# Performance work log

Measured on AMD Instinct MI355X. Metric: run time of the kernel, lower is better.

Reference implementation:

```python
import jax, jax.numpy as jnp
import numpy as np

B, N, C = 16, 1024, 768
H, HD = 9, 64  # num_active_heads, head_dim


def setup_inputs() -> dict:
    key = jax.random.key(0)
    ks = jax.random.split(key, 5)
    x = jax.random.normal(ks[0], (B, N, C), dtype=jnp.float32)
    qkv_w = jax.random.normal(ks[1], (3 * H * HD, C), dtype=jnp.float32) * (1.0 / np.sqrt(C))
    qkv_b = jax.random.normal(ks[2], (3 * H * HD,), dtype=jnp.float32) * 0.02
    proj_w = jax.random.normal(ks[3], (C, H * HD), dtype=jnp.float32) * (1.0 / np.sqrt(H * HD))
    proj_b = jax.random.normal(ks[4], (C,), dtype=jnp.float32) * 0.02
    return {"x": x, "qkv_w": qkv_w, "qkv_b": qkv_b, "proj_w": proj_w, "proj_b": proj_b}


def reference(x, qkv_w, qkv_b, proj_w, proj_b):
    b, n, c = x.shape
    # qkv projection: [B,N,3*H*HD] -> [3,B,H,N,HD]
    qkv = (x @ qkv_w.T + qkv_b).reshape(b, n, 3, H, HD).transpose(2, 0, 3, 1, 4)
    q, k, v = qkv[0], qkv[1], qkv[2]
    scale = HD ** -0.5
    attn = jnp.einsum('bhqd,bhkd->bhqk', q, k) * scale  # [B,H,N,N]
    attn = jax.nn.softmax(attn, axis=-1)
    out = jnp.einsum('bhqk,bhkd->bhqd', attn, v)  # [B,H,N,HD]
    out = out.transpose(0, 2, 1, 3).reshape(b, n, H * HD)
    return out @ proj_w.T + proj_b
```

## Files before the change

### kernel.cpp

```cpp
#include <hip/hip_runtime.h>


typedef _Float16 f16x8 __attribute__((ext_vector_type(8)));
typedef _Float16 f16x4 __attribute__((ext_vector_type(4)));
typedef float    f32x4 __attribute__((ext_vector_type(4)));

#define MFMA16(a, b, c) __builtin_amdgcn_mfma_f32_16x16x32_f16(a, b, c, 0, 0, 0)

__global__ __launch_bounds__(256) void cvt_f32_f16(const float* __restrict__ src,
                                                   _Float16* __restrict__ dst,
                                                   int nsrc, int ntot) {
  const int i4 = (blockIdx.x * 256 + threadIdx.x) * 4;
  if (i4 >= ntot) return;
  f16x4 h;
  if (i4 + 4 <= nsrc) {
    const float4 v = *(const float4*)(src + i4);
    ((_Float16*)&h)[0] = (_Float16)v.x;
    ((_Float16*)&h)[1] = (_Float16)v.y;
    ((_Float16*)&h)[2] = (_Float16)v.z;
    ((_Float16*)&h)[3] = (_Float16)v.w;
  } else {
    #pragma unroll
    for (int j = 0; j < 4; ++j) {
      const float v = (i4 + j < nsrc) ? src[i4 + j] : 0.f;
      ((_Float16*)&h)[j] = (_Float16)v;
    }
  }
  *(f16x4*)(dst + i4) = h;
}

__global__ __launch_bounds__(256, 2) void gemm1_qkv(const _Float16* __restrict__ A,
                                                    const _Float16* __restrict__ Bw,
                                                    const float* __restrict__ bias,
                                                    _Float16* __restrict__ Qo,
                                                    _Float16* __restrict__ Ko,
                                                    _Float16* __restrict__ Vt) {
  __shared__ __align__(16) _Float16 As[128 * 72];
  __shared__ __align__(16) _Float16 Bs[128 * 72];
  const int tid = threadIdx.x;
  const int wave = tid >> 6, lane = tid & 63;
  const int lo = lane & 15, hi = lane >> 4;
  const int wm = (wave >> 1) * 64, wn = (wave & 1) * 64;
  const int m0 = blockIdx.x * 128, n0 = blockIdx.y * 128;
  f32x4 acc[4][4] = {};
  for (int k0 = 0; k0 < 768; k0 += 64) {
    __syncthreads();
    #pragma unroll
    for (int it = 0; it < 4; ++it) {
      const int c = it * 256 + tid;
      const int row = c >> 3, cc = c & 7;
      *(uint4*)(As + row * 72 + cc * 8) = *(const uint4*)(A + (m0 + row) * 768 + k0 + cc * 8);
      *(uint4*)(Bs + row * 72 + cc * 8) = *(const uint4*)(Bw + (n0 + row) * 768 + k0 + cc * 8);
    }
    __syncthreads();
    #pragma unroll
    for (int ks = 0; ks < 2; ++ks) {
      f16x8 af[4], bf[4];
      #pragma unroll
      for (int t = 0; t < 4; ++t) {
        af[t] = *(const f16x8*)(As + (wm + t * 16 + lo) * 72 + ks * 32 + hi * 8);
        bf[t] = *(const f16x8*)(Bs + (wn + t * 16 + lo) * 72 + ks * 32 + hi * 8);
      }
      #pragma unroll
      for (int mt = 0; mt < 4; ++mt)
        #pragma unroll
        for (int nt = 0; nt < 4; ++nt)
          acc[mt][nt] = MFMA16(af[mt], bf[nt], acc[mt][nt]);
    }
  }
  const int b = m0 >> 10;
  const int nrbase = (m0 & 1023) + wm;
  #pragma unroll
  for (int nt = 0; nt < 4; ++nt) {
    const int n = n0 + wn + nt * 16 + lo;
    if (n < 1728) {
      const float bv = bias[n];
      const int t3 = n / 576;
      const int rem = n - t3 * 576;
      const int hh = rem >> 6, d = rem & 63;
      if (t3 == 2) {
        _Float16* dv = Vt + ((b * 9 + hh) << 16) + d * 1024;
        #pragma unroll
        for (int mt = 0; mt < 4; ++mt) {
          const int nr = nrbase + mt * 16 + hi * 4;
          f16x4 h4;
          #pragma unroll
          for (int i = 0; i < 4; ++i)
            ((_Float16*)&h4)[i] = (_Float16)(acc[mt][nt][i] + bv);
          *(f16x4*)(dv + nr) = h4;
        }
      } else {
        _Float16* dst = (t3 == 0 ? Qo : Ko) + ((b * 9 + hh) << 16) + d;
        #pragma unroll
        for (int mt = 0; mt < 4; ++mt) {
          const int nr = nrbase + mt * 16 + hi * 4;
          #pragma unroll
          for (int i = 0; i < 4; ++i)
            dst[(nr + i) * 64] = (_Float16)(acc[mt][nt][i] + bv);
        }
      }
    }
  }
}

__global__ __launch_bounds__(256, 3) void attn_fused(const _Float16* __restrict__ Qg,
                                                     const _Float16* __restrict__ Kg,
                                                     const _Float16* __restrict__ Vtg,
                                                     _Float16* __restrict__ Og) {
  __shared__ __align__(16) _Float16 Ks[128 * 72];
  __shared__ __align__(16) _Float16 Vts[64 * 136];
  __shared__ __align__(16) _Float16 QPs[4][16 * 136];
  const int tid = threadIdx.x;
  const int wave = tid >> 6, lane = tid & 63;
  const int lo = lane & 15, hi = lane >> 4;
  const int bh = blockIdx.x;
  const int q0 = blockIdx.y * 64;
  const _Float16* Qp  = Qg + (bh << 16);
  const _Float16* Kp  = Kg + (bh << 16);
  const _Float16* Vtp = Vtg + (bh << 16);

  {
    _Float16* Qs = &QPs[0][0];
    #pragma unroll
    for (int it = 0; it < 2; ++it) {
      const int c = it * 256 + tid;
      const int row = c >> 3, cc = c & 7;
      *(uint4*)(Qs + row * 72 + cc * 8) = *(const uint4*)(Qp + (q0 + row) * 64 + cc * 8);
    }
  }
  __syncthreads();
  f16x8 qf[2];
  #pragma unroll
  for (int ks = 0; ks < 2; ++ks)
    qf[ks] = *(const f16x8*)(&QPs[0][0] + (wave * 16 + lo) * 72 + ks * 32 + hi * 8);

  float m_run = -1e30f, l_run = 0.f;
  f32x4 accO[4] = {};
  const float cs = 0.125f * 1.44269504f;

  for (int t0 = 0; t0 < 1024; t0 += 128) {
    __syncthreads();
    #pragma unroll
    for (int it = 0; it < 4; ++it) {
      const int c = it * 256 + tid;
      const int row = c >> 3, cc = c & 7;
      *(uint4*)(Ks + row * 72 + cc * 8) = *(const uint4*)(Kp + (t0 + row) * 64 + cc * 8);
    }
    #pragma unroll
    for (int it = 0; it < 4; ++it) {
      const int c = it * 256 + tid;
      const int dr = c >> 4, c16 = c & 15;
      *(uint4*)(Vts + dr * 136 + c16 * 8) = *(const uint4*)(Vtp + dr * 1024 + t0 + c16 * 8);
    }
    __syncthreads();

    f32x4 sacc[8] = {};
    #pragma unroll
    for (int tt = 0; tt < 8; ++tt)
      #pragma unroll
      for (int ks = 0; ks < 2; ++ks) {
        const f16x8 kf = *(const f16x8*)(Ks + (tt * 16 + lo) * 72 + ks * 32 + hi * 8);
        sacc[tt] = MFMA16(kf, qf[ks], sacc[tt]);
      }

    float rmax = -1e30f;
    #pragma unroll
    for (int tt = 0; tt < 8; ++tt)
      #pragma unroll
      for (int i = 0; i < 4; ++i)
        rmax = fmaxf(rmax, sacc[tt][i]);
    rmax = fmaxf(rmax, __shfl_xor(rmax, 16, 64));
    rmax = fmaxf(rmax, __shfl_xor(rmax, 32, 64));
    const float mnew = fmaxf(m_run, rmax * cs);
    const float alpha = exp2f(m_run - mnew);
    float rsum = 0.f;
    #pragma unroll
    for (int tt = 0; tt < 8; ++tt) {
      f16x4 ph;
      #pragma unroll
      for (int i = 0; i < 4; ++i) {
        const float p = exp2f(fmaf(sacc[tt][i], cs, -mnew));
        rsum += p;
        ((_Float16*)&ph)[i] = (_Float16)p;
      }
      *(f16x4*)(&QPs[wave][lo * 136 + tt * 16 + hi * 4]) = ph;
    }
    rsum += __shfl_xor(rsum, 16, 64);
    rsum += __shfl_xor(rsum, 32, 64);
    l_run = l_run * alpha + rsum;
    m_run = mnew;
    #pragma unroll
    for (int dt = 0; dt < 4; ++dt) accO[dt] *= alpha;

    #pragma unroll
    for (int ks2 = 0; ks2 < 4; ++ks2) {
      const f16x8 pf = *(const f16x8*)(&QPs[wave][lo * 136 + ks2 * 32 + hi * 8]);
      #pragma unroll
      for (int dt = 0; dt < 4; ++dt) {
        const f16x8 vf = *(const f16x8*)(Vts + (dt * 16 + lo) * 136 + ks2 * 32 + hi * 8);
        accO[dt] = MFMA16(vf, pf, accO[dt]);
      }
    }
  }
  const float inv = 1.f / l_run;
  const int qrow = q0 + wave * 16 + lo;
  const int b = bh / 9, hh = bh - (bh / 9) * 9;
  _Float16* op = Og + (((b << 10) + qrow) * 576 + hh * 64);
  #pragma unroll
  for (int dt = 0; dt < 4; ++dt) {
    f16x4 o4;
    #pragma unroll
    for (int i = 0; i < 4; ++i)
      ((_Float16*)&o4)[i] = (_Float16)(accO[dt][i] * inv);
    *(f16x4*)(op + dt * 16 + hi * 4) = o4;
  }
}

__global__ __launch_bounds__(256, 2) void gemm3_proj(const _Float16* __restrict__ A,
                                                     const _Float16* __restrict__ Bw,
                                                     const float* __restrict__ bias,
                                                     float* __restrict__ out) {
  __shared__ __align__(16) _Float16 As[128 * 72];
  __shared__ __align__(16) _Float16 Bs[128 * 72];
  const int tid = threadIdx.x;
  const int wave = tid >> 6, lane = tid & 63;
  const int lo = lane & 15, hi = lane >> 4;
  const int wm = (wave >> 1) * 64, wn = (wave & 1) * 64;
  const int m0 = blockIdx.x * 128, n0 = blockIdx.y * 128;
  f32x4 acc[4][4] = {};
  for (int k0 = 0; k0 < 576; k0 += 64) {
    __syncthreads();
    #pragma unroll
    for (int it = 0; it < 4; ++it) {
      const int c = it * 256 + tid;
      const int row = c >> 3, cc = c & 7;
      *(uint4*)(As + row * 72 + cc * 8) = *(const uint4*)(A + (m0 + row) * 576 + k0 + cc * 8);
      *(uint4*)(Bs + row * 72 + cc * 8) = *(const uint4*)(Bw + (n0 + row) * 576 + k0 + cc * 8);
    }
    __syncthreads();
    #pragma unroll
    for (int ks = 0; ks < 2; ++ks) {
      f16x8 af[4], bf[4];
      #pragma unroll
      for (int t = 0; t < 4; ++t) {
        af[t] = *(const f16x8*)(As + (wm + t * 16 + lo) * 72 + ks * 32 + hi * 8);
        bf[t] = *(const f16x8*)(Bs + (wn + t * 16 + lo) * 72 + ks * 32 + hi * 8);
      }
      #pragma unroll
      for (int mt = 0; mt < 4; ++mt)
        #pragma unroll
        for (int nt = 0; nt < 4; ++nt)
          acc[mt][nt] = MFMA16(af[mt], bf[nt], acc[mt][nt]);
    }
  }
  #pragma unroll
  for (int nt = 0; nt < 4; ++nt) {
    const int n = n0 + wn + nt * 16 + lo;
    const float bv = bias[n];
    #pragma unroll
    for (int mt = 0; mt < 4; ++mt) {
      const int mrow = m0 + wm + mt * 16 + hi * 4;
      #pragma unroll
      for (int i = 0; i < 4; ++i)
        out[(mrow + i) * 768 + n] = acc[mt][nt][i] + bv;
    }
  }
}

extern "C" void kernel_launch(void* const* d_in, const int* in_sizes, int n_in,
                              void* d_out, int out_size, void* d_ws, size_t ws_size,
                              hipStream_t stream) {
  const float* x      = (const float*)d_in[0];
  const float* qkv_w  = (const float*)d_in[1];
  const float* qkv_b  = (const float*)d_in[2];
  const float* proj_w = (const float*)d_in[3];
  const float* proj_b = (const float*)d_in[4];
  float* out = (float*)d_out;

  char* ws = (char*)d_ws;
  _Float16* x16 = (_Float16*)(ws + 0);
  _Float16* w1p = (_Float16*)(ws + 25165824);
  _Float16* w2h = (_Float16*)(ws + 27918336);
  _Float16* Qh  = (_Float16*)(ws + 28803072);
  _Float16* Kh  = (_Float16*)(ws + 47677440);
  _Float16* Vth = (_Float16*)(ws + 66551808);
  _Float16* Oh  = (_Float16*)(ws + 85426176);

  cvt_f32_f16<<<12288, 256, 0, stream>>>(x, x16, 12582912, 12582912);
  cvt_f32_f16<<<1344, 256, 0, stream>>>(qkv_w, w1p, 1327104, 1376256);
  cvt_f32_f16<<<432, 256, 0, stream>>>(proj_w, w2h, 442368, 442368);
  gemm1_qkv<<<dim3(128, 14), 256, 0, stream>>>(x16, w1p, qkv_b, Qh, Kh, Vth);
  attn_fused<<<dim3(144, 16), 256, 0, stream>>>(Qh, Kh, Vth, Oh);
  gemm3_proj<<<dim3(128, 6), 256, 0, stream>>>(Oh, w2h, proj_b, out);
}
```

Measured before the change: 271.2 us.

## Use direct global-to-LDS loads with XOR-swizzled layouts instead of padded shared tiles

Replaces register-staged global-to-shared copies in all three compute kernels with global_load_lds DMA into unpadded tiles. Because that path cannot pad rows, producers (conversion kernel, QKV epilogue, attention output) now write data in an XOR-swizzled chunk order, and readers un-swizzle on LDS access to avoid bank conflicts. Attention drops the separate P buffer by reusing the K tile, which needs an extra barrier. Occupancy hints rise to 4, and conversions use packed round-toward-zero f16 plus native exp2. Costs are more complex index math, an added sync per tile, and rounding-mode changes.

Result: faster. 257.2 us (-5.2%).

```diff
diff --git a/kernel.cpp b/kernel.cpp
--- a/kernel.cpp
+++ b/kernel.cpp
@@ -3,40 +3,47 @@
 
 typedef _Float16 f16x8 __attribute__((ext_vector_type(8)));
 typedef _Float16 f16x4 __attribute__((ext_vector_type(4)));
+typedef __fp16   h16x2 __attribute__((ext_vector_type(2)));
 typedef float    f32x4 __attribute__((ext_vector_type(4)));
 
 #define MFMA16(a, b, c) __builtin_amdgcn_mfma_f32_16x16x32_f16(a, b, c, 0, 0, 0)
 
-__global__ __launch_bounds__(256) void cvt_f32_f16(const float* __restrict__ src,
-                                                   _Float16* __restrict__ dst,
-                                                   int nsrc, int ntot) {
-  const int i4 = (blockIdx.x * 256 + threadIdx.x) * 4;
-  if (i4 >= ntot) return;
-  f16x4 h;
-  if (i4 + 4 <= nsrc) {
-    const float4 v = *(const float4*)(src + i4);
-    ((_Float16*)&h)[0] = (_Float16)v.x;
-    ((_Float16*)&h)[1] = (_Float16)v.y;
-    ((_Float16*)&h)[2] = (_Float16)v.z;
-    ((_Float16*)&h)[3] = (_Float16)v.w;
+__device__ __forceinline__ void gld16(const _Float16* g, _Float16* l) {
+  __builtin_amdgcn_global_load_lds((const __attribute__((address_space(1))) void*)g,
+                                   (__attribute__((address_space(3))) void*)l, 16, 0, 0);
+}
+
+__global__ __launch_bounds__(256) void cvt_swz(const float* __restrict__ src,
+                                               _Float16* __restrict__ dst,
+                                               int rows_src, int cpr, int total) {
+  const int g = blockIdx.x * 256 + threadIdx.x;
+  if (g >= total) return;
+  const int row = g / cpr;
+  const int c = g - row * cpr;
+  const int L = cpr * 8;
+  const int pos = (c & ~7) | ((c ^ row) & 7);
+  union { f16x8 v; h16x2 h[4]; } u;
+  if (row < rows_src) {
+    const float4 a = *(const float4*)(src + row * L + c * 8);
+    const float4 b = *(const float4*)(src + row * L + c * 8 + 4);
+    u.h[0] = __builtin_amdgcn_cvt_pkrtz(a.x, a.y);
+    u.h[1] = __builtin_amdgcn_cvt_pkrtz(a.z, a.w);
+    u.h[2] = __builtin_amdgcn_cvt_pkrtz(b.x, b.y);
+    u.h[3] = __builtin_amdgcn_cvt_pkrtz(b.z, b.w);
   } else {
-    #pragma unroll
-    for (int j = 0; j < 4; ++j) {
-      const float v = (i4 + j < nsrc) ? src[i4 + j] : 0.f;
-      ((_Float16*)&h)[j] = (_Float16)v;
-    }
-  }
-  *(f16x4*)(dst + i4) = h;
-}
-
-__global__ __launch_bounds__(256, 2) void gemm1_qkv(const _Float16* __restrict__ A,
+    u.v = (f16x8){};
+  }
+  *(f16x8*)(dst + row * L + pos * 8) = u.v;
+}
+
+__global__ __launch_bounds__(256, 4) void gemm1_qkv(const _Float16* __restrict__ A,
                                                     const _Float16* __restrict__ Bw,
                                                     const float* __restrict__ bias,
                                                     _Float16* __restrict__ Qo,
                                                     _Float16* __restrict__ Ko,
                                                     _Float16* __restrict__ Vt) {
-  __shared__ __align__(16) _Float16 As[128 * 72];
-  __shared__ __align__(16) _Float16 Bs[128 * 72];
+  __shared__ __align__(16) _Float16 As[128 * 64];
+  __shared__ __align__(16) _Float16 Bs[128 * 64];
   const int tid = threadIdx.x;
   const int wave = tid >> 6, lane = tid & 63;
   const int lo = lane & 15, hi = lane >> 4;
@@ -46,20 +53,21 @@
   for (int k0 = 0; k0 < 768; k0 += 64) {
     __syncthreads();
     #pragma unroll
-    for (int it = 0; it < 4; ++it) {
-      const int c = it * 256 + tid;
-      const int row = c >> 3, cc = c & 7;
-      *(uint4*)(As + row * 72 + cc * 8) = *(const uint4*)(A + (m0 + row) * 768 + k0 + cc * 8);
-      *(uint4*)(Bs + row * 72 + cc * 8) = *(const uint4*)(Bw + (n0 + row) * 768 + k0 + cc * 8);
+    for (int j = 0; j < 4; ++j) {
+      const int seg = wave * 4 + j;
+      const int gr = seg * 8 + (lane >> 3), gc = (lane & 7) << 3;
+      gld16(A + (m0 + gr) * 768 + k0 + gc, As + seg * 512);
+      gld16(Bw + (n0 + gr) * 768 + k0 + gc, Bs + seg * 512);
     }
     __syncthreads();
     #pragma unroll
     for (int ks = 0; ks < 2; ++ks) {
       f16x8 af[4], bf[4];
+      const int p = ((ks * 4 + hi) ^ (lo & 7)) << 3;
       #pragma unroll
       for (int t = 0; t < 4; ++t) {
-        af[t] = *(const f16x8*)(As + (wm + t * 16 + lo) * 72 + ks * 32 + hi * 8);
-        bf[t] = *(const f16x8*)(Bs + (wn + t * 16 + lo) * 72 + ks * 32 + hi * 8);
+        af[t] = *(const f16x8*)(As + (wm + t * 16 + lo) * 64 + p);
+        bf[t] = *(const f16x8*)(Bs + (wn + t * 16 + lo) * 64 + p);
       }
       #pragma unroll
       for (int mt = 0; mt < 4; ++mt)
@@ -78,38 +86,51 @@
       const int t3 = n / 576;
       const int rem = n - t3 * 576;
       const int hh = rem >> 6, d = rem & 63;
+      const int bh16 = (b * 9 + hh) << 16;
       if (t3 == 2) {
-        _Float16* dv = Vt + ((b * 9 + hh) << 16) + d * 1024;
+        _Float16* dv = Vt + bh16 + d * 1024;
         #pragma unroll
         for (int mt = 0; mt < 4; ++mt) {
           const int nr = nrbase + mt * 16 + hi * 4;
-          f16x4 h4;
+          const int c = nr >> 3;
+          const int pos = (c & ~7) | ((c ^ d) & 7);
+          union { f16x4 v; h16x2 h[2]; } u;
+          u.h[0] = __builtin_amdgcn_cvt_pkrtz(acc[mt][nt][0] + bv, acc[mt][nt][1] + bv);
+          u.h[1] = __builtin_amdgcn_cvt_pkrtz(acc[mt][nt][2] + bv, acc[mt][nt][3] + bv);
+          *(f16x4*)(dv + pos * 8 + (nr & 7)) = u.v;
+        }
+      } else if (t3 == 1) {
+        _Float16* dk = Ko + bh16;
+        const int ch = d >> 3, dl = d & 7;
+        #pragma unroll
+        for (int mt = 0; mt < 4; ++mt) {
+          const int nr = nrbase + mt * 16 + hi * 4;
           #pragma unroll
-          for (int i = 0; i < 4; ++i)
-            ((_Float16*)&h4)[i] = (_Float16)(acc[mt][nt][i] + bv);
-          *(f16x4*)(dv + nr) = h4;
+          for (int i = 0; i < 4; ++i) {
+            const int t = nr + i;
+            dk[t * 64 + ((ch ^ (t & 7)) << 3) + dl] = (_Float16)(acc[mt][nt][i] + bv);
+          }
         }
       } else {
-        _Float16* dst = (t3 == 0 ? Qo : Ko) + ((b * 9 + hh) << 16) + d;
+        _Float16* dq = Qo + bh16 + d;
         #pragma unroll
         for (int mt = 0; mt < 4; ++mt) {
           const int nr = nrbase + mt * 16 + hi * 4;
           #pragma unroll
           for (int i = 0; i < 4; ++i)
-            dst[(nr + i) * 64] = (_Float16)(acc[mt][nt][i] + bv);
+            dq[(nr + i) * 64] = (_Float16)(acc[mt][nt][i] + bv);
         }
       }
     }
   }
 }
 
-__global__ __launch_bounds__(256, 3) void attn_fused(const _Float16* __restrict__ Qg,
+__global__ __launch_bounds__(256, 4) void attn_fused(const _Float16* __restrict__ Qg,
                                                      const _Float16* __restrict__ Kg,
                                                      const _Float16* __restrict__ Vtg,
                                                      _Float16* __restrict__ Og) {
-  __shared__ __align__(16) _Float16 Ks[128 * 72];
-  __shared__ __align__(16) _Float16 Vts[64 * 136];
-  __shared__ __align__(16) _Float16 QPs[4][16 * 136];
+  __shared__ __align__(16) _Float16 Ks[128 * 64];
+  __shared__ __align__(16) _Float16 Vts[64 * 128];
   const int tid = threadIdx.x;
   const int wave = tid >> 6, lane = tid & 63;
   const int lo = lane & 15, hi = lane >> 4;
@@ -119,21 +140,20 @@
   const _Float16* Kp  = Kg + (bh << 16);
   const _Float16* Vtp = Vtg + (bh << 16);
 
-  {
-    _Float16* Qs = &QPs[0][0];
-    #pragma unroll
-    for (int it = 0; it < 2; ++it) {
-      const int c = it * 256 + tid;
-      const int row = c >> 3, cc = c & 7;
-      *(uint4*)(Qs + row * 72 + cc * 8) = *(const uint4*)(Qp + (q0 + row) * 64 + cc * 8);
-    }
+  #pragma unroll
+  for (int it = 0; it < 2; ++it) {
+    const int c = it * 256 + tid;
+    const int row = c >> 3, ch = c & 7;
+    *(uint4*)(Ks + row * 64 + ((ch ^ (row & 7)) << 3)) =
+        *(const uint4*)(Qp + (q0 + row) * 64 + ch * 8);
   }
   __syncthreads();
   f16x8 qf[2];
   #pragma unroll
   for (int ks = 0; ks < 2; ++ks)
-    qf[ks] = *(const f16x8*)(&QPs[0][0] + (wave * 16 + lo) * 72 + ks * 32 + hi * 8);
-
+    qf[ks] = *(const f16x8*)(Ks + (wave * 16 + lo) * 64 + (((ks * 4 + hi) ^ (lo & 7)) << 3));
+
+  _Float16* Ps = Ks + wave * 2048;
   float m_run = -1e30f, l_run = 0.f;
   f32x4 accO[4] = {};
   const float cs = 0.125f * 1.44269504f;
@@ -141,16 +161,10 @@
   for (int t0 = 0; t0 < 1024; t0 += 128) {
     __syncthreads();
     #pragma unroll
-    for (int it = 0; it < 4; ++it) {
-      const int c = it * 256 + tid;
-      const int row = c >> 3, cc = c & 7;
-      *(uint4*)(Ks + row * 72 + cc * 8) = *(const uint4*)(Kp + (t0 + row) * 64 + cc * 8);
-    }
-    #pragma unroll
-    for (int it = 0; it < 4; ++it) {
-      const int c = it * 256 + tid;
-      const int dr = c >> 4, c16 = c & 15;
-      *(uint4*)(Vts + dr * 136 + c16 * 8) = *(const uint4*)(Vtp + dr * 1024 + t0 + c16 * 8);
+    for (int j = 0; j < 4; ++j) {
+      const int seg = wave * 4 + j;
+      gld16(Kp + (t0 + seg * 8 + (lane >> 3)) * 64 + ((lane & 7) << 3), Ks + seg * 512);
+      gld16(Vtp + (seg * 4 + (lane >> 4)) * 1024 + t0 + ((lane & 15) << 3), Vts + seg * 512);
     }
     __syncthreads();
 
@@ -159,31 +173,32 @@
     for (int tt = 0; tt < 8; ++tt)
       #pragma unroll
       for (int ks = 0; ks < 2; ++ks) {
-        const f16x8 kf = *(const f16x8*)(Ks + (tt * 16 + lo) * 72 + ks * 32 + hi * 8);
+        const f16x8 kf = *(const f16x8*)(Ks + (tt * 16 + lo) * 64 + (((ks * 4 + hi) ^ (lo & 7)) << 3));
         sacc[tt] = MFMA16(kf, qf[ks], sacc[tt]);
       }
+    __syncthreads();
 
     float rmax = -1e30f;
     #pragma unroll
     for (int tt = 0; tt < 8; ++tt)
-      #pragma unroll
-      for (int i = 0; i < 4; ++i)
-        rmax = fmaxf(rmax, sacc[tt][i]);
+      rmax = fmaxf(rmax, fmaxf(fmaxf(sacc[tt][0], sacc[tt][1]), fmaxf(sacc[tt][2], sacc[tt][3])));
     rmax = fmaxf(rmax, __shfl_xor(rmax, 16, 64));
     rmax = fmaxf(rmax, __shfl_xor(rmax, 32, 64));
     const float mnew = fmaxf(m_run, rmax * cs);
-    const float alpha = exp2f(m_run - mnew);
+    const float alpha = __builtin_amdgcn_exp2f(m_run - mnew);
     float rsum = 0.f;
     #pragma unroll
     for (int tt = 0; tt < 8; ++tt) {
-      f16x4 ph;
-      #pragma unroll
-      for (int i = 0; i < 4; ++i) {
-        const float p = exp2f(fmaf(sacc[tt][i], cs, -mnew));
-        rsum += p;
-        ((_Float16*)&ph)[i] = (_Float16)p;
-      }
-      *(f16x4*)(&QPs[wave][lo * 136 + tt * 16 + hi * 4]) = ph;
+      const float p0 = __builtin_amdgcn_exp2f(fmaf(sacc[tt][0], cs, -mnew));
+      const float p1 = __builtin_amdgcn_exp2f(fmaf(sacc[tt][1], cs, -mnew));
+      const float p2 = __builtin_amdgcn_exp2f(fmaf(sacc[tt][2], cs, -mnew));
+      const float p3 = __builtin_amdgcn_exp2f(fmaf(sacc[tt][3], cs, -mnew));
+      rsum += (p0 + p1) + (p2 + p3);
+      union { f16x4 v; h16x2 h[2]; } u;
+      u.h[0] = __builtin_amdgcn_cvt_pkrtz(p0, p1);
+      u.h[1] = __builtin_amdgcn_cvt_pkrtz(p2, p3);
+      const int c = 2 * tt + (hi >> 1);
+      *(f16x4*)(Ps + lo * 128 + (((c & 8) | ((c ^ lo) & 7)) << 3) + ((hi & 1) << 2)) = u.v;
     }
     rsum += __shfl_xor(rsum, 16, 64);
     rsum += __shfl_xor(rsum, 32, 64);
@@ -194,34 +209,36 @@
 
     #pragma unroll
     for (int ks2 = 0; ks2 < 4; ++ks2) {
-      const f16x8 pf = *(const f16x8*)(&QPs[wave][lo * 136 + ks2 * 32 + hi * 8]);
+      const int c = 4 * ks2 + hi;
+      const f16x8 pf = *(const f16x8*)(Ps + lo * 128 + (((c & 8) | ((c ^ lo) & 7)) << 3));
       #pragma unroll
       for (int dt = 0; dt < 4; ++dt) {
-        const f16x8 vf = *(const f16x8*)(Vts + (dt * 16 + lo) * 136 + ks2 * 32 + hi * 8);
+        const int dd = dt * 16 + lo;
+        const f16x8 vf = *(const f16x8*)(Vts + dd * 128 + (((c & 8) | ((c ^ dd) & 7)) << 3));
         accO[dt] = MFMA16(vf, pf, accO[dt]);
       }
     }
   }
   const float inv = 1.f / l_run;
-  const int qrow = q0 + wave * 16 + lo;
-  const int b = bh / 9, hh = bh - (bh / 9) * 9;
-  _Float16* op = Og + (((b << 10) + qrow) * 576 + hh * 64);
+  const int b = bh / 9, hh = bh - b * 9;
+  const int rq = (b << 10) + q0 + wave * 16 + lo;
   #pragma unroll
   for (int dt = 0; dt < 4; ++dt) {
-    f16x4 o4;
-    #pragma unroll
-    for (int i = 0; i < 4; ++i)
-      ((_Float16*)&o4)[i] = (_Float16)(accO[dt][i] * inv);
-    *(f16x4*)(op + dt * 16 + hi * 4) = o4;
-  }
-}
-
-__global__ __launch_bounds__(256, 2) void gemm3_proj(const _Float16* __restrict__ A,
+    union { f16x4 v; h16x2 h[2]; } u;
+    u.h[0] = __builtin_amdgcn_cvt_pkrtz(accO[dt][0] * inv, accO[dt][1] * inv);
+    u.h[1] = __builtin_amdgcn_cvt_pkrtz(accO[dt][2] * inv, accO[dt][3] * inv);
+    const int c = hh * 8 + dt * 2 + (hi >> 1);
+    const int pos = (c & ~7) | ((c ^ rq) & 7);
+    *(f16x4*)(Og + rq * 576 + pos * 8 + ((hi & 1) << 2)) = u.v;
+  }
+}
+
+__global__ __launch_bounds__(256, 4) void gemm3_proj(const _Float16* __restrict__ A,
                                                      const _Float16* __restrict__ Bw,
                                                      const float* __restrict__ bias,
                                                      float* __restrict__ out) {
-  __shared__ __align__(16) _Float16 As[128 * 72];
-  __shared__ __align__(16) _Float16 Bs[128 * 72];
+  __shared__ __align__(16) _Float16 As[128 * 64];
+  __shared__ __align__(16) _Float16 Bs[128 * 64];
   const int tid = threadIdx.x;
   const int wave = tid >> 6, lane = tid & 63;
   const int lo = lane & 15, hi = lane >> 4;
@@ -231,20 +248,21 @@
   for (int k0 = 0; k0 < 576; k0 += 64) {
     __syncthreads();
     #pragma unroll
-    for (int it = 0; it < 4; ++it) {
-      const int c = it * 256 + tid;
-      const int row = c >> 3, cc = c & 7;
-      *(uint4*)(As + row * 72 + cc * 8) = *(const uint4*)(A + (m0 + row) * 576 + k0 + cc * 8);
-      *(uint4*)(Bs + row * 72 + cc * 8) = *(const uint4*)(Bw + (n0 + row) * 576 + k0 + cc * 8);
+    for (int j = 0; j < 4; ++j) {
+      const int seg = wave * 4 + j;
+      const int gr = seg * 8 + (lane >> 3), gc = (lane & 7) << 3;
+      gld16(A + (m0 + gr) * 576 + k0 + gc, As + seg * 512);
+      gld16(Bw + (n0 + gr) * 576 + k0 + gc, Bs + seg * 512);
     }
     __syncthreads();
     #pragma unroll
     for (int ks = 0; ks < 2; ++ks) {
       f16x8 af[4], bf[4];
+      const int p = ((ks * 4 + hi) ^ (lo & 7)) << 3;
       #pragma unroll
       for (int t = 0; t < 4; ++t) {
-        af[t] = *(const f16x8*)(As + (wm + t * 16 + lo) * 72 + ks * 32 + hi * 8);
-        bf[t] = *(const f16x8*)(Bs + (wn + t * 16 + lo) * 72 + ks * 32 + hi * 8);
+        af[t] = *(const f16x8*)(As + (wm + t * 16 + lo) * 64 + p);
+        bf[t] = *(const f16x8*)(Bs + (wn + t * 16 + lo) * 64 + p);
       }
       #pragma unroll
       for (int mt = 0; mt < 4; ++mt)
@@ -286,9 +304,9 @@
   _Float16* Vth = (_Float16*)(ws + 66551808);
   _Float16* Oh  = (_Float16*)(ws + 85426176);
 
-  cvt_f32_f16<<<12288, 256, 0, stream>>>(x, x16, 12582912, 12582912);
-  cvt_f32_f16<<<1344, 256, 0, stream>>>(qkv_w, w1p, 1327104, 1376256);
-  cvt_f32_f16<<<432, 256, 0, stream>>>(proj_w, w2h, 442368, 442368);
+  cvt_swz<<<6144, 256, 0, stream>>>(x, x16, 16384, 96, 16384 * 96);
+  cvt_swz<<<672, 256, 0, stream>>>(qkv_w, w1p, 1728, 96, 1792 * 96);
+  cvt_swz<<<216, 256, 0, stream>>>(proj_w, w2h, 768, 72, 768 * 72);
   gemm1_qkv<<<dim3(128, 14), 256, 0, stream>>>(x16, w1p, qkv_b, Qh, Kh, Vth);
   attn_fused<<<dim3(144, 16), 256, 0, stream>>>(Qh, Kh, Vth, Oh);
   gemm3_proj<<<dim3(128, 6), 256, 0, stream>>>(Oh, w2h, proj_b, out);
```
